# Kernel optimization log

Measured on AMD Instinct MI355X. Metric: run time of the kernel, lower is better.

Reference implementation:

```python
import jax, jax.numpy as jnp
import numpy as np

PC_RANGE = (-51.2, -51.2, -5.0, 51.2, 51.2, 3.0)
E, CAMS, LVLS = 256, 6, 4
LVL_HW = [(64, 176), (32, 88), (16, 44), (8, 22)]


def setup_inputs() -> dict:
    key = jax.random.key(0)
    ks = jax.random.split(key, 16)
    B, N = 2, 6400
    inp = {
        'instance_feature': jax.random.normal(ks[0], (B, N, E), jnp.float32),
        'anchor': jax.random.normal(ks[1], (B, N, 11), jnp.float32),
        'projection': jax.random.uniform(ks[2], (B, CAMS, 4, 4), jnp.float32),
    }
    for i, (H, W) in enumerate(LVL_HW):
        inp[f'feat{i}'] = jax.random.normal(ks[3 + i], (B, CAMS, E, H, W), jnp.float32)
    # learned params (random, not the zero-init of the module, to exercise the math)
    inp['attn_w'] = jax.random.normal(ks[8], (CAMS * LVLS, E), jnp.float32) * 0.02
    inp['attn_b'] = jax.random.normal(ks[9], (CAMS * LVLS,), jnp.float32) * 0.02
    inp['vp_w'] = jax.random.normal(ks[10], (E, E), jnp.float32) * (1.0 / np.sqrt(E))
    inp['vp_b'] = jnp.zeros((E,), jnp.float32)
    inp['op_w'] = jax.random.normal(ks[11], (E, E), jnp.float32) * (1.0 / np.sqrt(E))
    inp['op_b'] = jnp.zeros((E,), jnp.float32)
    return inp


def _bilinear_sample(feat, x, y):
    """feat: [BN, C, H, W]; x, y: [BN, N] pixel coords.
    Bilinear, zeros padding, align_corners=True (pixel coords == uv directly).
    Returns [BN, N, C]."""
    BN, C, H, W = feat.shape
    x0 = jnp.floor(x); y0 = jnp.floor(y)
    wx1 = x - x0; wx0 = 1.0 - wx1
    wy1 = y - y0; wy0 = 1.0 - wy1
    feat_flat = feat.reshape(BN, C, H * W)
    b = jnp.arange(BN)[:, None]

    def corner(xi, yi, w):
        valid = (xi >= 0) & (xi <= W - 1) & (yi >= 0) & (yi <= H - 1)
        xi_c = jnp.clip(xi, 0, W - 1).astype(jnp.int32)
        yi_c = jnp.clip(yi, 0, H - 1).astype(jnp.int32)
        idx = yi_c * W + xi_c                      # [BN, N]
        v = feat_flat[b, :, idx]                   # [BN, N, C]
        return v * (w * valid.astype(w.dtype))[..., None]

    return (corner(x0, y0, wx0 * wy0) + corner(x0 + 1, y0, wx1 * wy0)
            + corner(x0, y0 + 1, wx0 * wy1) + corner(x0 + 1, y0 + 1, wx1 * wy1))


def reference(instance_feature, anchor, projection, feat0, feat1, feat2, feat3,
              attn_w, attn_b, vp_w, vp_b, op_w, op_b):
    B, N, _ = instance_feature.shape
    feats = [feat0, feat1, feat2, feat3]
    # attention weights over cams x levels (softmax over levels, dim=-1)
    attn = (instance_feature @ attn_w.T + attn_b).reshape(B, N, CAMS, LVLS)
    attn = jax.nn.softmax(attn, axis=-1)
    # anchor center -> world coords
    xyz = jax.nn.sigmoid(anchor[..., :3])
    pr = jnp.asarray(PC_RANGE, dtype=anchor.dtype)
    xyz_world = xyz * (pr[3:6] - pr[0:3]) + pr[0:3]
    xyz_h = jnp.concatenate([xyz_world, jnp.ones((B, N, 1), anchor.dtype)], axis=-1)
    xyz_cam = jnp.einsum('bcij,bnj->bcni', projection, xyz_h)   # [B,CAMS,N,4]
    depth = jnp.maximum(xyz_cam[..., 2:3], 1e-4)
    uv = xyz_cam[..., :2] / depth                               # [B,CAMS,N,2] pixel coords
    BN = B * CAMS
    x = uv[..., 0].reshape(BN, N)
    y = uv[..., 1].reshape(BN, N)
    sampled = []
    for feat in feats:
        H, W = feat.shape[-2], feat.shape[-1]
        s = _bilinear_sample(feat.reshape(BN, E, H, W), x, y)   # [BN,N,E]
        sampled.append(s.reshape(B, CAMS, N, E))
    S = jnp.stack(sampled, axis=0)                              # [L,B,CAMS,N,E]
    out = jnp.einsum('lbcne,bncl->bne', S, attn)
    out = out @ vp_w.T + vp_b
    out = (out + instance_feature) @ op_w.T + op_b
    return out
```

## Files before the change

kernel.cpp:

```cpp
#include <hip/hip_runtime.h>
#include <hip/hip_fp16.h>
#include <math.h>

#define B_ 2
#define N_ 6400
#define E_ 256
#define C_ 6
#define L_ 4
#define SL2_ 128

__device__ __host__ constexpr int HWH[4] = {64, 32, 16, 8};
__device__ __host__ constexpr int HWW[4] = {176, 88, 44, 22};
__device__ __host__ constexpr int LOFF[4] = {0, 11264, 14080, 14784};
#define HWT 14960

typedef __attribute__((ext_vector_type(8))) _Float16 half8;
typedef __attribute__((ext_vector_type(4))) float floatx4;

__global__ __launch_bounds__(256) void prep_kernel(
    const float* __restrict__ inst, const float* __restrict__ anchor,
    const float* __restrict__ proj, const float* __restrict__ attn_w,
    const float* __restrict__ attn_b,
    uint4* __restrict__ meta_w, int4* __restrict__ meta_b)
{
    __shared__ float AWT[256 * 24];
    __shared__ float ts[256 * 33];

    const int tid = threadIdx.x;

    for (int idx = tid; idx < 24 * 256; idx += 256) {
        int j = idx >> 8, k = idx & 255;
        AWT[k * 24 + j] = attn_w[idx];
    }
    __syncthreads();

    const int pt0 = blockIdx.x * 256;

    float acc[24];
#pragma unroll
    for (int j = 0; j < 24; j++) acc[j] = attn_b[j];

    for (int k0 = 0; k0 < 256; k0 += 32) {
#pragma unroll
        for (int r = 0; r < 32; r++) {
            int lin = r * 256 + tid;
            int p = lin >> 5, kk = lin & 31;
            ts[p * 33 + kk] = inst[(size_t)(pt0 + p) * 256 + k0 + kk];
        }
        __syncthreads();
#pragma unroll
        for (int kk = 0; kk < 32; kk++) {
            float v = ts[tid * 33 + kk];
            const float* aw = &AWT[(k0 + kk) * 24];
#pragma unroll
            for (int j = 0; j < 24; j++) acc[j] += v * aw[j];
        }
        __syncthreads();
    }

    const int pt = pt0 + tid;
    const int b = pt / N_;
    const int n = pt - b * N_;

    float attn[24];
#pragma unroll
    for (int c = 0; c < C_; c++) {
        float m = fmaxf(fmaxf(acc[c * 4], acc[c * 4 + 1]),
                        fmaxf(acc[c * 4 + 2], acc[c * 4 + 3]));
        float s = 0.f;
#pragma unroll
        for (int l = 0; l < L_; l++) {
            float e = expf(acc[c * 4 + l] - m);
            attn[c * 4 + l] = e;
            s += e;
        }
        float r = 1.f / s;
#pragma unroll
        for (int l = 0; l < L_; l++) attn[c * 4 + l] *= r;
    }

    float ax = anchor[(size_t)pt * 11 + 0];
    float ay = anchor[(size_t)pt * 11 + 1];
    float az = anchor[(size_t)pt * 11 + 2];
    float wxp = (1.f / (1.f + expf(-ax))) * 102.4f - 51.2f;
    float wyp = (1.f / (1.f + expf(-ay))) * 102.4f - 51.2f;
    float wzp = (1.f / (1.f + expf(-az))) * 8.f - 5.f;

#pragma unroll
    for (int c = 0; c < C_; c++) {
        const float* P = &proj[(size_t)(b * C_ + c) * 16];
        float cx = P[0] * wxp + P[1] * wyp + P[2] * wzp + P[3];
        float cy = P[4] * wxp + P[5] * wyp + P[6] * wzp + P[7];
        float cz = P[8] * wxp + P[9] * wyp + P[10] * wzp + P[11];
        float d = fmaxf(cz, 1e-4f);
        float u = cx / d, v = cy / d;

        float x0f = floorf(u), y0f = floorf(v);
        float fx1 = u - x0f, fy1 = v - y0f;
        float fx0 = 1.f - fx1, fy0 = 1.f - fy1;

        float4 wl[4]; int bsx[4];
#pragma unroll
        for (int l = 0; l < L_; l++) {
            const int W = HWW[l], H = HWH[l];
            float ax0, ax1; int bx;
            int ix = (int)fminf(fmaxf(x0f, -2.f), (float)W);
            if (ix <= -2 || ix >= W)      { ax0 = 0.f;  ax1 = 0.f;  bx = 0; }
            else if (ix == -1)            { ax0 = fx1;  ax1 = 0.f;  bx = 0; }
            else if (ix == W - 1)         { ax0 = 0.f;  ax1 = fx0;  bx = W - 2; }
            else                          { ax0 = fx0;  ax1 = fx1;  bx = ix; }
            float ay0, ay1; int by;
            int iy = (int)fminf(fmaxf(y0f, -2.f), (float)H);
            if (iy <= -2 || iy >= H)      { ay0 = 0.f;  ay1 = 0.f;  by = 0; }
            else if (iy == -1)            { ay0 = fy1;  ay1 = 0.f;  by = 0; }
            else if (iy == H - 1)         { ay0 = 0.f;  ay1 = fy0;  by = H - 2; }
            else                          { ay0 = fy0;  ay1 = fy1;  by = iy; }

            float a = attn[c * 4 + l];
            wl[l] = make_float4(a * ay0 * ax0, a * ay0 * ax1,
                                a * ay1 * ax0, a * ay1 * ax1);
            bsx[l] = by * W + bx;
        }
        size_t mi = (size_t)(b * C_ + c) * N_ + n;
        union { uint4 u; __half2 h[4]; } q0, q1;
        q0.h[0] = __floats2half2_rn(wl[0].x, wl[0].y);
        q0.h[1] = __floats2half2_rn(wl[0].z, wl[0].w);
        q0.h[2] = __floats2half2_rn(wl[1].x, wl[1].y);
        q0.h[3] = __floats2half2_rn(wl[1].z, wl[1].w);
        q1.h[0] = __floats2half2_rn(wl[2].x, wl[2].y);
        q1.h[1] = __floats2half2_rn(wl[2].z, wl[2].w);
        q1.h[2] = __floats2half2_rn(wl[3].x, wl[3].y);
        q1.h[3] = __floats2half2_rn(wl[3].z, wl[3].w);
        meta_w[mi * 2 + 0] = q0.u;
        meta_w[mi * 2 + 1] = q1.u;
        meta_b[mi] = make_int4(bsx[0], bsx[1], bsx[2], bsx[3]);
    }
}

template<bool PART>
__global__ __launch_bounds__(1024) void gather_t(
    const float* __restrict__ f0, const float* __restrict__ f1,
    const float* __restrict__ f2, const float* __restrict__ f3,
    const uint4* __restrict__ meta_w, const int4* __restrict__ meta_b,
    __half2* __restrict__ part2, float* __restrict__ agg)
{
    __shared__ __half2 lds2[HWT];

    const int tid = threadIdx.x;
    int bid = blockIdx.x;
    bid = (bid & 7) * 192 + (bid >> 3);
    const int slice = bid & 127;
    const int c = (bid >> 7) % C_;
    const int b = bid / (128 * C_);
    const int e0 = slice * 2;
    const int bc = b * C_ + c;

    const float* fs[4] = {f0, f1, f2, f3};

#pragma unroll
    for (int l = 0; l < L_; l++) {
        const int HW = HWH[l] * HWW[l];
        const float* s0 = fs[l] + (size_t)(bc * E_ + e0) * HW;
        const float* s1 = s0 + HW;
        const int quarter = HW >> 2;
        for (int q = tid; q < quarter; q += 1024) {
            int p = q * 4;
            float4 v0 = *(const float4*)(s0 + p);
            float4 v1 = *(const float4*)(s1 + p);
            union { uint4 u; __half2 h[4]; } pk;
            pk.h[0] = __floats2half2_rn(v0.x, v1.x);
            pk.h[1] = __floats2half2_rn(v0.y, v1.y);
            pk.h[2] = __floats2half2_rn(v0.z, v1.z);
            pk.h[3] = __floats2half2_rn(v0.w, v1.w);
            *(uint4*)&lds2[LOFF[l] + p] = pk.u;
        }
    }
    __syncthreads();

    const size_t mbase = (size_t)bc * N_;
    const uint4* mwp = meta_w + mbase * 2;
    const int4* mbp = meta_b + mbase;
    __half2* pout = part2 + ((size_t)bc * SL2_ + slice) * N_;
    float* aggb = agg + (size_t)b * N_ * E_ + e0;

    int n = tid;
    uint4 m0, m1; int4 px;
    uint4 o0, o1; int4 ox;
    {
        m0 = mwp[(size_t)n * 2];
        m1 = mwp[(size_t)n * 2 + 1];
        px = mbp[n];
    }
    if (n + 1024 < N_) {
        o0 = mwp[(size_t)(n + 1024) * 2];
        o1 = mwp[(size_t)(n + 1024) * 2 + 1];
        ox = mbp[n + 1024];
    }

    while (n < N_) {
        const int n2 = n + 2048;
        uint4 t0, t1; int4 tx;
        if (n2 < N_) {
            t0 = mwp[(size_t)n2 * 2];
            t1 = mwp[(size_t)n2 * 2 + 1];
            tx = mbp[n2];
        }

        union { uint4 u; __half2 h[4]; } a0u, a1u;
        a0u.u = m0; a1u.u = m1;
        float4 ws[4];
        {
            float2 p0 = __half22float2(a0u.h[0]), p1 = __half22float2(a0u.h[1]);
            float2 p2 = __half22float2(a0u.h[2]), p3 = __half22float2(a0u.h[3]);
            ws[0] = make_float4(p0.x, p0.y, p1.x, p1.y);
            ws[1] = make_float4(p2.x, p2.y, p3.x, p3.y);
            float2 p4 = __half22float2(a1u.h[0]), p5 = __half22float2(a1u.h[1]);
            float2 p6 = __half22float2(a1u.h[2]), p7 = __half22float2(a1u.h[3]);
            ws[2] = make_float4(p4.x, p4.y, p5.x, p5.y);
            ws[3] = make_float4(p6.x, p6.y, p7.x, p7.y);
        }
        const int pxs[4] = {px.x, px.y, px.z, px.w};

        float a0 = 0.f, a1 = 0.f;
#pragma unroll
        for (int l = 0; l < L_; l++) {
            float4 w = ws[l];
            if (w.x != 0.f || w.y != 0.f || w.z != 0.f || w.w != 0.f) {
                const int W = HWW[l];
                const int base = LOFF[l] + pxs[l];
                float2 f00 = __half22float2(lds2[base]);
                float2 f01 = __half22float2(lds2[base + 1]);
                float2 f10 = __half22float2(lds2[base + W]);
                float2 f11 = __half22float2(lds2[base + W + 1]);
                a0 += w.x * f00.x + w.y * f01.x + w.z * f10.x + w.w * f11.x;
                a1 += w.x * f00.y + w.y * f01.y + w.z * f10.y + w.w * f11.y;
            }
        }

        if (PART) {
            pout[n] = __floats2half2_rn(a0, a1);
        } else {
            if (a0 != 0.f || a1 != 0.f) {
                float* dst = aggb + (size_t)n * E_;
                atomicAdd(dst + 0, a0);
                atomicAdd(dst + 1, a1);
            }
        }

        n += 1024;
        m0 = o0; m1 = o1; px = ox;
        o0 = t0; o1 = t1; ox = tx;
    }
}

#define SAS2 264
#define WSS2 72
#define KC 64

__global__ __launch_bounds__(512) void gemm_mfma(
    const float* __restrict__ inst,
    const float* __restrict__ vp_w, const float* __restrict__ vp_b,
    const float* __restrict__ op_w, const float* __restrict__ op_b,
    const __half2* __restrict__ part2, float* __restrict__ out)
{
    __shared__ _Float16 sA[64 * SAS2];
    __shared__ _Float16 sT[64 * SAS2];
    __shared__ _Float16 wS[256 * WSS2];

    const int tid = threadIdx.x;
    const int wave = tid >> 6;
    const int lane = tid & 63;
    const int mt = wave & 3;
    const int nh = wave >> 2;
    const int q = lane >> 4;
    const int col = lane & 15;

    const int p0 = blockIdx.x * 64;
    const int b = p0 / N_;
    const int nbase = p0 - b * N_;

    {
        const int p = tid & 63, sg = tid >> 6;
        const int n = nbase + p;
        for (int s = sg; s < SL2_; s += 8) {
            float a0 = 0.f, a1 = 0.f;
#pragma unroll
            for (int c = 0; c < C_; c++) {
                float2 f = __half22float2(
                    part2[((size_t)(b * C_ + c) * SL2_ + s) * N_ + n]);
                a0 += f.x; a1 += f.y;
            }
            sA[p * SAS2 + s * 2 + 0] = (_Float16)a0;
            sA[p * SAS2 + s * 2 + 1] = (_Float16)a1;
        }
    }

    floatx4 acc[8];
#pragma unroll
    for (int nt = 0; nt < 8; nt++) acc[nt] = (floatx4)(0.f);

    for (int kc = 0; kc < 256 / KC; kc++) {
        __syncthreads();
        {
            const int row = tid >> 1, half = tid & 1;
            const float* src = vp_w + (size_t)row * 256 + kc * KC + half * 32;
            _Float16* dst = &wS[row * WSS2 + half * 32];
#pragma unroll
            for (int i = 0; i < 4; i++) {
                float4 v = *(const float4*)(src + i * 8);
                float4 u = *(const float4*)(src + i * 8 + 4);
                half8 h = {(_Float16)v.x, (_Float16)v.y, (_Float16)v.z, (_Float16)v.w,
                           (_Float16)u.x, (_Float16)u.y, (_Float16)u.z, (_Float16)u.w};
                *(half8*)(dst + i * 8) = h;
            }
        }
        __syncthreads();
#pragma unroll
        for (int ks = 0; ks < KC / 32; ks++) {
            half8 a = *(half8*)&sA[(mt * 16 + col) * SAS2 + kc * KC + ks * 32 + q * 8];
#pragma unroll
            for (int nt = 0; nt < 8; nt++) {
                half8 bf = *(half8*)&wS[(nh * 128 + nt * 16 + col) * WSS2 + ks * 32 + q * 8];
                acc[nt] = __builtin_amdgcn_mfma_f32_16x16x32_f16(a, bf, acc[nt], 0, 0, 0);
            }
        }
    }

#pragma unroll
    for (int nt = 0; nt < 8; nt++) {
        const int e = nh * 128 + nt * 16 + col;
        const float bv = vp_b[e];
#pragma unroll
        for (int r = 0; r < 4; r++) {
            const int p = mt * 16 + q * 4 + r;
            float t = acc[nt][r] + bv + inst[(size_t)(p0 + p) * E_ + e];
            sT[p * SAS2 + e] = (_Float16)t;
        }
        acc[nt] = (floatx4)(0.f);
    }

    for (int kc = 0; kc < 256 / KC; kc++) {
        __syncthreads();
        {
            const int row = tid >> 1, half = tid & 1;
            const float* src = op_w + (size_t)row * 256 + kc * KC + half * 32;
            _Float16* dst = &wS[row * WSS2 + half * 32];
#pragma unroll
            for (int i = 0; i < 4; i++) {
                float4 v = *(const float4*)(src + i * 8);
                float4 u = *(const float4*)(src + i * 8 + 4);
                half8 h = {(_Float16)v.x, (_Float16)v.y, (_Float16)v.z, (_Float16)v.w,
                           (_Float16)u.x, (_Float16)u.y, (_Float16)u.z, (_Float16)u.w};
                *(half8*)(dst + i * 8) = h;
            }
        }
        __syncthreads();
#pragma unroll
        for (int ks = 0; ks < KC / 32; ks++) {
            half8 a = *(half8*)&sT[(mt * 16 + col) * SAS2 + kc * KC + ks * 32 + q * 8];
#pragma unroll
            for (int nt = 0; nt < 8; nt++) {
                half8 bf = *(half8*)&wS[(nh * 128 + nt * 16 + col) * WSS2 + ks * 32 + q * 8];
                acc[nt] = __builtin_amdgcn_mfma_f32_16x16x32_f16(a, bf, acc[nt], 0, 0, 0);
            }
        }
    }

#pragma unroll
    for (int nt = 0; nt < 8; nt++) {
        const int e = nh * 128 + nt * 16 + col;
        const float ob = op_b[e];
#pragma unroll
        for (int r = 0; r < 4; r++) {
            const int p = mt * 16 + q * 4 + r;
            out[(size_t)(p0 + p) * E_ + e] = acc[nt][r] + ob;
        }
    }
}

#define PT 32
#define SAS 264
#define WSS 36

__global__ __launch_bounds__(256) void gemm_valu(
    const float* __restrict__ inst,
    const float* __restrict__ vp_w, const float* __restrict__ vp_b,
    const float* __restrict__ op_w, const float* __restrict__ op_b,
    float* __restrict__ io)
{
    __shared__ __align__(16) float sA[PT * SAS];
    __shared__ __align__(16) float wS[256 * WSS];

    const int tid = threadIdx.x;
    const int eg = tid & 31;
    const int pg = tid >> 5;
    const int p0 = blockIdx.x * PT;

#pragma unroll
    for (int r = 0; r < PT; r++)
        sA[r * SAS + tid] = io[(size_t)(p0 + r) * E_ + tid];
    __syncthreads();

    float acc[4][8];
#pragma unroll
    for (int j = 0; j < 4; j++)
#pragma unroll
        for (int i = 0; i < 8; i++) acc[j][i] = 0.f;

    for (int k0 = 0; k0 < 256; k0 += 32) {
        __syncthreads();
#pragma unroll
        for (int r = 0; r < 32; r++) {
            int lin = r * 256 + tid;
            int e = lin >> 5, kk = lin & 31;
            wS[e * WSS + kk] = vp_w[(size_t)e * 256 + k0 + kk];
        }
        __syncthreads();
#pragma unroll
        for (int kk = 0; kk < 32; kk += 4) {
            float4 wv4[8], av4[4];
#pragma unroll
            for (int i = 0; i < 8; i++)
                wv4[i] = *(const float4*)&wS[(eg + 32 * i) * WSS + kk];
#pragma unroll
            for (int j = 0; j < 4; j++)
                av4[j] = *(const float4*)&sA[(pg * 4 + j) * SAS + k0 + kk];
#pragma unroll
            for (int j = 0; j < 4; j++)
#pragma unroll
                for (int i = 0; i < 8; i++)
                    acc[j][i] += av4[j].x * wv4[i].x + av4[j].y * wv4[i].y
                               + av4[j].z * wv4[i].z + av4[j].w * wv4[i].w;
        }
    }

    __syncthreads();
#pragma unroll
    for (int j = 0; j < 4; j++) {
        int p = pg * 4 + j;
#pragma unroll
        for (int i = 0; i < 8; i++) {
            int e = eg + 32 * i;
            float t = acc[j][i] + vp_b[e] + inst[(size_t)(p0 + p) * E_ + e];
            sA[p * SAS + e] = t;
            acc[j][i] = 0.f;
        }
    }

    for (int k0 = 0; k0 < 256; k0 += 32) {
        __syncthreads();
#pragma unroll
        for (int r = 0; r < 32; r++) {
            int lin = r * 256 + tid;
            int e = lin >> 5, kk = lin & 31;
            wS[e * WSS + kk] = op_w[(size_t)e * 256 + k0 + kk];
        }
        __syncthreads();
#pragma unroll
        for (int kk = 0; kk < 32; kk += 4) {
            float4 wv4[8], av4[4];
#pragma unroll
            for (int i = 0; i < 8; i++)
                wv4[i] = *(const float4*)&wS[(eg + 32 * i) * WSS + kk];
#pragma unroll
            for (int j = 0; j < 4; j++)
                av4[j] = *(const float4*)&sA[(pg * 4 + j) * SAS + k0 + kk];
#pragma unroll
            for (int j = 0; j < 4; j++)
#pragma unroll
                for (int i = 0; i < 8; i++)
                    acc[j][i] += av4[j].x * wv4[i].x + av4[j].y * wv4[i].y
                               + av4[j].z * wv4[i].z + av4[j].w * wv4[i].w;
        }
    }

#pragma unroll
    for (int j = 0; j < 4; j++) {
        int p = pg * 4 + j;
#pragma unroll
        for (int i = 0; i < 8; i++) {
            int e = eg + 32 * i;
            io[(size_t)(p0 + p) * E_ + e] = acc[j][i] + op_b[e];
        }
    }
}

extern "C" void kernel_launch(void* const* d_in, const int* in_sizes, int n_in,
                              void* d_out, int out_size, void* d_ws, size_t ws_size,
                              hipStream_t stream)
{
    const float* inst   = (const float*)d_in[0];
    const float* anchor = (const float*)d_in[1];
    const float* proj   = (const float*)d_in[2];
    const float* f0     = (const float*)d_in[3];
    const float* f1     = (const float*)d_in[4];
    const float* f2     = (const float*)d_in[5];
    const float* f3     = (const float*)d_in[6];
    const float* attn_w = (const float*)d_in[7];
    const float* attn_b = (const float*)d_in[8];
    const float* vp_w   = (const float*)d_in[9];
    const float* vp_b   = (const float*)d_in[10];
    const float* op_w   = (const float*)d_in[11];
    const float* op_b   = (const float*)d_in[12];
    float* out = (float*)d_out;

    const size_t NPT = (size_t)B_ * C_ * N_;
    uint4* meta_w = (uint4*)d_ws;
    int4* meta_b = (int4*)((char*)d_ws + NPT * 32);
    __half2* part2 = (__half2*)((char*)d_ws + NPT * 48);
    const size_t part2_bytes = (size_t)B_ * C_ * SL2_ * N_ * sizeof(__half2);
    const size_t need = NPT * 48 + part2_bytes;

    prep_kernel<<<(B_ * N_) / 256, 256, 0, stream>>>(
        inst, anchor, proj, attn_w, attn_b, meta_w, meta_b);

    if (ws_size >= need) {
        gather_t<true><<<B_ * C_ * SL2_, 1024, 0, stream>>>(
            f0, f1, f2, f3, meta_w, meta_b, part2, out);
        gemm_mfma<<<(B_ * N_) / 64, 512, 0, stream>>>(
            inst, vp_w, vp_b, op_w, op_b, part2, out);
    } else {
        hipMemsetAsync(d_out, 0, (size_t)out_size * sizeof(float), stream);
        gather_t<false><<<B_ * C_ * SL2_, 1024, 0, stream>>>(
            f0, f1, f2, f3, meta_w, meta_b, part2, out);
        gemm_valu<<<(B_ * N_) / PT, 256, 0, stream>>>(
            inst, vp_w, vp_b, op_w, op_b, out);
    }
}
```

Before: 348.8 us.

## Make gather loop branchless and double GEMM row tile with shared LDS buffer

The gather inner loop drops the per-level zero-weight branch and computes all four level contributions unconditionally, summing them as a tree. This removes divergence at the cost of always doing the LDS reads. The GEMM kernel now processes 128 rows per block with 1024 threads. It reuses a single LDS buffer for the input and intermediate tiles, adding a barrier before the overwrite, and splits the weight staging across four threads per row. The larger tile amortises each weight-tile load over twice as many rows, but it halves the block count to 100 and may reduce occupancy.

```diff
diff --git a/kernel.cpp b/kernel.cpp
--- a/kernel.cpp
+++ b/kernel.cpp
@@ -208,34 +208,30 @@
 
         union { uint4 u; __half2 h[4]; } a0u, a1u;
         a0u.u = m0; a1u.u = m1;
-        float4 ws[4];
-        {
-            float2 p0 = __half22float2(a0u.h[0]), p1 = __half22float2(a0u.h[1]);
-            float2 p2 = __half22float2(a0u.h[2]), p3 = __half22float2(a0u.h[3]);
-            ws[0] = make_float4(p0.x, p0.y, p1.x, p1.y);
-            ws[1] = make_float4(p2.x, p2.y, p3.x, p3.y);
-            float2 p4 = __half22float2(a1u.h[0]), p5 = __half22float2(a1u.h[1]);
-            float2 p6 = __half22float2(a1u.h[2]), p7 = __half22float2(a1u.h[3]);
-            ws[2] = make_float4(p4.x, p4.y, p5.x, p5.y);
-            ws[3] = make_float4(p6.x, p6.y, p7.x, p7.y);
-        }
+        __half2 wh[8];
+        wh[0] = a0u.h[0]; wh[1] = a0u.h[1]; wh[2] = a0u.h[2]; wh[3] = a0u.h[3];
+        wh[4] = a1u.h[0]; wh[5] = a1u.h[1]; wh[6] = a1u.h[2]; wh[7] = a1u.h[3];
+
         const int pxs[4] = {px.x, px.y, px.z, px.w};
 
-        float a0 = 0.f, a1 = 0.f;
+        float p0[4], p1[4];
 #pragma unroll
         for (int l = 0; l < L_; l++) {
-            float4 w = ws[l];
-            if (w.x != 0.f || w.y != 0.f || w.z != 0.f || w.w != 0.f) {
-                const int W = HWW[l];
-                const int base = LOFF[l] + pxs[l];
-                float2 f00 = __half22float2(lds2[base]);
-                float2 f01 = __half22float2(lds2[base + 1]);
-                float2 f10 = __half22float2(lds2[base + W]);
-                float2 f11 = __half22float2(lds2[base + W + 1]);
-                a0 += w.x * f00.x + w.y * f01.x + w.z * f10.x + w.w * f11.x;
-                a1 += w.x * f00.y + w.y * f01.y + w.z * f10.y + w.w * f11.y;
-            }
-        }
+            const int W = HWW[l];
+            const int base = LOFF[l] + pxs[l];
+            float2 wab = __half22float2(wh[l * 2]);
+            float2 wcd = __half22float2(wh[l * 2 + 1]);
+            float2 f00 = __half22float2(lds2[base]);
+            float2 f01 = __half22float2(lds2[base + 1]);
+            float2 f10 = __half22float2(lds2[base + W]);
+            float2 f11 = __half22float2(lds2[base + W + 1]);
+            p0[l] = (wab.x * f00.x + wab.y * f01.x)
+                  + (wcd.x * f10.x + wcd.y * f11.x);
+            p1[l] = (wab.x * f00.y + wab.y * f01.y)
+                  + (wcd.x * f10.y + wcd.y * f11.y);
+        }
+        float a0 = (p0[0] + p0[1]) + (p0[2] + p0[3]);
+        float a1 = (p1[0] + p1[1]) + (p1[2] + p1[3]);
 
         if (PART) {
             pout[n] = __floats2half2_rn(a0, a1);
@@ -257,30 +253,29 @@
 #define WSS2 72
 #define KC 64
 
-__global__ __launch_bounds__(512) void gemm_mfma(
+__global__ __launch_bounds__(1024, 4) void gemm_mfma(
     const float* __restrict__ inst,
     const float* __restrict__ vp_w, const float* __restrict__ vp_b,
     const float* __restrict__ op_w, const float* __restrict__ op_b,
     const __half2* __restrict__ part2, float* __restrict__ out)
 {
-    __shared__ _Float16 sA[64 * SAS2];
-    __shared__ _Float16 sT[64 * SAS2];
+    __shared__ _Float16 sA[128 * SAS2];
     __shared__ _Float16 wS[256 * WSS2];
 
     const int tid = threadIdx.x;
     const int wave = tid >> 6;
     const int lane = tid & 63;
-    const int mt = wave & 3;
-    const int nh = wave >> 2;
+    const int mt = wave & 7;
+    const int nh = wave >> 3;
     const int q = lane >> 4;
     const int col = lane & 15;
 
-    const int p0 = blockIdx.x * 64;
+    const int p0 = blockIdx.x * 128;
     const int b = p0 / N_;
     const int nbase = p0 - b * N_;
 
     {
-        const int p = tid & 63, sg = tid >> 6;
+        const int p = tid & 127, sg = tid >> 7;
         const int n = nbase + p;
         for (int s = sg; s < SL2_; s += 8) {
             float a0 = 0.f, a1 = 0.f;
@@ -302,11 +297,11 @@
     for (int kc = 0; kc < 256 / KC; kc++) {
         __syncthreads();
         {
-            const int row = tid >> 1, half = tid & 1;
-            const float* src = vp_w + (size_t)row * 256 + kc * KC + half * 32;
-            _Float16* dst = &wS[row * WSS2 + half * 32];
-#pragma unroll
-            for (int i = 0; i < 4; i++) {
+            const int row = tid >> 2, qt = tid & 3;
+            const float* src = vp_w + (size_t)row * 256 + kc * KC + qt * 16;
+            _Float16* dst = &wS[row * WSS2 + qt * 16];
+#pragma unroll
+            for (int i = 0; i < 2; i++) {
                 float4 v = *(const float4*)(src + i * 8);
                 float4 u = *(const float4*)(src + i * 8 + 4);
                 half8 h = {(_Float16)v.x, (_Float16)v.y, (_Float16)v.z, (_Float16)v.w,
@@ -326,6 +321,7 @@
         }
     }
 
+    __syncthreads();
 #pragma unroll
     for (int nt = 0; nt < 8; nt++) {
         const int e = nh * 128 + nt * 16 + col;
@@ -334,7 +330,7 @@
         for (int r = 0; r < 4; r++) {
             const int p = mt * 16 + q * 4 + r;
             float t = acc[nt][r] + bv + inst[(size_t)(p0 + p) * E_ + e];
-            sT[p * SAS2 + e] = (_Float16)t;
+            sA[p * SAS2 + e] = (_Float16)t;
         }
         acc[nt] = (floatx4)(0.f);
     }
@@ -342,11 +338,11 @@
     for (int kc = 0; kc < 256 / KC; kc++) {
         __syncthreads();
         {
-            const int row = tid >> 1, half = tid & 1;
-            const float* src = op_w + (size_t)row * 256 + kc * KC + half * 32;
-            _Float16* dst = &wS[row * WSS2 + half * 32];
-#pragma unroll
-            for (int i = 0; i < 4; i++) {
+            const int row = tid >> 2, qt = tid & 3;
+            const float* src = op_w + (size_t)row * 256 + kc * KC + qt * 16;
+            _Float16* dst = &wS[row * WSS2 + qt * 16];
+#pragma unroll
+            for (int i = 0; i < 2; i++) {
                 float4 v = *(const float4*)(src + i * 8);
                 float4 u = *(const float4*)(src + i * 8 + 4);
                 half8 h = {(_Float16)v.x, (_Float16)v.y, (_Float16)v.z, (_Float16)v.w,
@@ -357,7 +353,7 @@
         __syncthreads();
 #pragma unroll
         for (int ks = 0; ks < KC / 32; ks++) {
-            half8 a = *(half8*)&sT[(mt * 16 + col) * SAS2 + kc * KC + ks * 32 + q * 8];
+            half8 a = *(half8*)&sA[(mt * 16 + col) * SAS2 + kc * KC + ks * 32 + q * 8];
 #pragma unroll
             for (int nt = 0; nt < 8; nt++) {
                 half8 bf = *(half8*)&wS[(nh * 128 + nt * 16 + col) * WSS2 + ks * 32 + q * 8];
@@ -517,7 +513,7 @@
     if (ws_size >= need) {
         gather_t<true><<<B_ * C_ * SL2_, 1024, 0, stream>>>(
             f0, f1, f2, f3, meta_w, meta_b, part2, out);
-        gemm_mfma<<<(B_ * N_) / 64, 512, 0, stream>>>(
+        gemm_mfma<<<(B_ * N_) / 128, 1024, 0, stream>>>(
             inst, vp_w, vp_b, op_w, op_b, part2, out);
     } else {
         hipMemsetAsync(d_out, 0, (size_t)out_size * sizeof(float), stream);
```

New measurement: 345.6 us. No clear change (-0.9%).
